# Performance work log

Measured on AMD Instinct MI355X. Metric: run time of the kernel, lower is better.

The kernel has to match this reference:

```python
import jax, jax.numpy as jnp
import numpy as np

B, LQ, LK, D, H = 2, 1024, 1024, 1024, 16
DH = D // H


def setup_inputs() -> dict:
    key = jax.random.key(0)
    ks = jax.random.split(key, 14)
    s = 1.0 / np.sqrt(D)
    inp = {
        "q": jax.random.normal(ks[0], (B, LQ, D), jnp.float32),
        "k": jax.random.normal(ks[1], (B, LK, D), jnp.float32),
        "v": jax.random.normal(ks[2], (B, LK, D), jnp.float32),
        "Wq": jax.random.normal(ks[3], (D, D), jnp.float32) * s,
        "bq": jnp.zeros((D,), jnp.float32),
        "Wk": jax.random.normal(ks[4], (D, D), jnp.float32) * s,
        "bk": jnp.zeros((D,), jnp.float32),
        "Wv": jax.random.normal(ks[5], (D, D), jnp.float32) * s,
        "bv": jnp.zeros((D,), jnp.float32),
        "Wo": jax.random.normal(ks[6], (D, D), jnp.float32) * s,
        "bo": jnp.zeros((D,), jnp.float32),
        "logits_bias": jax.random.normal(ks[7], (B, LQ, LK), jnp.float32),
        "key_padding_mask": jax.random.randint(ks[8], (B, LK), 0, 2) > 0,
    }
    return inp


def _split_heads(x):
    b, l, _ = x.shape
    return x.reshape(b, l, H, DH).transpose(0, 2, 1, 3)  # [B,H,L,DH]


def reference(q, k, v, Wq, bq, Wk, bk, Wv, bv, Wo, bo, logits_bias, key_padding_mask):
    qh = _split_heads(q @ Wq.T + bq)  # [B,H,Lq,DH]
    kh = _split_heads(k @ Wk.T + bk)  # [B,H,Lk,DH]
    vh = _split_heads(v @ Wv.T + bv)  # [B,H,Lk,DH]

    neg = jnp.finfo(qh.dtype).min
    # attn_mask = logits_bias broadcast over heads, masked_fill at padded keys
    attn_mask = jnp.where(key_padding_mask[:, None, None, :],
                          neg, logits_bias[:, None, :, :])  # [B,1,Lq,Lk]

    scale = 1.0 / np.sqrt(DH)
    scores = jnp.einsum('bhqd,bhkd->bhqk', qh, kh) * scale + attn_mask
    probs = jax.nn.softmax(scores, axis=-1)
    out = jnp.einsum('bhqk,bhkd->bhqd', probs, vh)  # [B,H,Lq,DH]
    out = out.transpose(0, 2, 1, 3).reshape(q.shape[0], q.shape[1], D)
    return out @ Wo.T + bo
```

## Files before the change

### kernel.cpp

```cpp
#include <hip/hip_runtime.h>


typedef _Float16 half8 __attribute__((ext_vector_type(8)));
typedef _Float16 half4_t __attribute__((ext_vector_type(4)));
typedef float f32x4 __attribute__((ext_vector_type(4)));

#define MFMA16(a, b, c) __builtin_amdgcn_mfma_f32_16x16x32_f16((a), (b), (c), 0, 0, 0)

#define WAITCNT_VM(n) asm volatile("s_waitcnt vmcnt(" #n ")" ::: "memory")
#define WAITCNT_LGKM0() asm volatile("s_waitcnt lgkmcnt(0)" ::: "memory")
#define RAW_BARRIER() asm volatile("s_barrier" ::: "memory")
#define EXP2F(x) __builtin_amdgcn_exp2f(x)

__device__ __forceinline__ void gload16(const void* g, void* l) {
  __builtin_amdgcn_global_load_lds(
      (const __attribute__((address_space(1))) unsigned int*)g,
      (__attribute__((address_space(3))) unsigned int*)l, 16, 0, 0);
}

__device__ __forceinline__ half8 frag_ld(const _Float16* t, int row, int ck) {
  return *(const half8*)(t + row * 64 + (((ck ^ (row & 7)) << 3)));
}

__global__ __launch_bounds__(256) void cvt_f32_f16(
    const float* __restrict__ q, const float* __restrict__ k, const float* __restrict__ v,
    const float* __restrict__ Wq, const float* __restrict__ Wk,
    const float* __restrict__ Wv, const float* __restrict__ Wo,
    const float* __restrict__ biasL, const int* __restrict__ kpm,
    _Float16* __restrict__ q16, _Float16* __restrict__ k16, _Float16* __restrict__ v16,
    _Float16* __restrict__ w16, _Float16* __restrict__ biasC) {
  const int y = blockIdx.y;
  if (y == 5) {
    const size_t i = ((size_t)blockIdx.x * 256 + threadIdx.x) * 8;
    const int b = (int)(i >> 20);
    const int kk = (int)(i & 1023);
    const int* mrow = kpm + (b << 10) + kk;
    const float4 b0 = *(const float4*)(biasL + i);
    const float4 b1 = *(const float4*)(biasL + i + 4);
    const int4 m0 = *(const int4*)mrow;
    const int4 m1 = *(const int4*)(mrow + 4);
    const float sc = 1.44269504f;
    half8 h;
    h[0] = m0.x ? (_Float16)-30000.f : (_Float16)(b0.x * sc - 8.f);
    h[1] = m0.y ? (_Float16)-30000.f : (_Float16)(b0.y * sc - 8.f);
    h[2] = m0.z ? (_Float16)-30000.f : (_Float16)(b0.z * sc - 8.f);
    h[3] = m0.w ? (_Float16)-30000.f : (_Float16)(b0.w * sc - 8.f);
    h[4] = m1.x ? (_Float16)-30000.f : (_Float16)(b1.x * sc - 8.f);
    h[5] = m1.y ? (_Float16)-30000.f : (_Float16)(b1.y * sc - 8.f);
    h[6] = m1.z ? (_Float16)-30000.f : (_Float16)(b1.z * sc - 8.f);
    h[7] = m1.w ? (_Float16)-30000.f : (_Float16)(b1.w * sc - 8.f);
    *(half8*)(biasC + i) = h;
    return;
  }
  const float* s;
  _Float16* d;
  const size_t M = (size_t)1024 * 1024;
  int x = blockIdx.x;
  switch (y) {
    case 0: s = q;  d = q16; break;
    case 1: s = k;  d = k16; break;
    case 2: s = v;  d = v16; break;
    case 3: if (x < 512) { s = Wq; d = w16; } else { s = Wk; d = w16 + M; x -= 512; } break;
    default: if (x < 512) { s = Wv; d = w16 + 2 * M; } else { s = Wo; d = w16 + 3 * M; x -= 512; } break;
  }
  const size_t i = ((size_t)x * 256 + threadIdx.x) * 8;
  const float4 a = *(const float4*)(s + i);
  const float4 bvv = *(const float4*)(s + i + 4);
  half8 h;
  h[0] = (_Float16)a.x; h[1] = (_Float16)a.y; h[2] = (_Float16)a.z; h[3] = (_Float16)a.w;
  h[4] = (_Float16)bvv.x; h[5] = (_Float16)bvv.y; h[6] = (_Float16)bvv.z; h[7] = (_Float16)bvv.w;
  *(half8*)(d + i) = h;
}

__global__ __launch_bounds__(256, 2) void mmp_big(
    const _Float16* __restrict__ Aq, const _Float16* __restrict__ Ak,
    const _Float16* __restrict__ Av, const _Float16* __restrict__ W16,
    const float* __restrict__ c0, const float* __restrict__ c1,
    const float* __restrict__ c2, _Float16* __restrict__ Dq,
    _Float16* __restrict__ Dk, _Float16* __restrict__ Dvt) {
  __shared__ __align__(16) _Float16 lds[32768];

  const int tid = threadIdx.x;
  const int wv = tid >> 6, ln = tid & 63;
  const int quad = ln >> 4, col = ln & 15;
  const int wm = wv >> 1, wn = wv & 1;
  const int n0 = blockIdx.x * 128;
  const int m0 = blockIdx.y * 128;
  const int z = blockIdx.z;
  const bool swapped = (z < 2);

  const _Float16* A = (z == 0) ? Aq : (z == 1) ? Ak : Av;
  const _Float16* Bw = W16 + (size_t)z * 1024 * 1024;
  const float* bias = (z == 0) ? c0 : (z == 1) ? c1 : c2;

  auto stage = [&](int buf, int k0) {
#pragma unroll
    for (int j = 0; j < 8; ++j) {
      const int ci = j * 256 + tid;
      const _Float16* src;
      if (ci < 1024) {
        const int row = ci >> 3, lc = (ci & 7) ^ (row & 7);
        src = A + (size_t)(m0 + row) * 1024 + k0 + lc * 8;
      } else {
        const int di = ci - 1024;
        const int row = di >> 3, lc = (di & 7) ^ (row & 7);
        src = Bw + (size_t)(n0 + row) * 1024 + k0 + lc * 8;
      }
      gload16(src, lds + buf * 16384 + (j * 256 + wv * 64) * 8);
    }
  };

  const f32x4 zero4 = {0.f, 0.f, 0.f, 0.f};
  f32x4 acc[4][4];
#pragma unroll
  for (int i = 0; i < 4; ++i)
#pragma unroll
    for (int j = 0; j < 4; ++j) acc[i][j] = zero4;

  auto kstep = [&](const _Float16* As, const _Float16* Bs) {
    half8 af0[4], bf0[4], af1[4], bf1[4];
#pragma unroll
    for (int mi = 0; mi < 4; ++mi) af0[mi] = frag_ld(As, wm * 64 + mi * 16 + col, quad);
#pragma unroll
    for (int ni = 0; ni < 4; ++ni) bf0[ni] = frag_ld(Bs, wn * 64 + ni * 16 + col, quad);
#pragma unroll
    for (int mi = 0; mi < 4; ++mi) af1[mi] = frag_ld(As, wm * 64 + mi * 16 + col, 4 + quad);
#pragma unroll
    for (int ni = 0; ni < 4; ++ni) bf1[ni] = frag_ld(Bs, wn * 64 + ni * 16 + col, 4 + quad);
    WAITCNT_LGKM0();
    RAW_BARRIER();
    if (swapped) {
#pragma unroll
      for (int ni = 0; ni < 4; ++ni)
#pragma unroll
        for (int mi = 0; mi < 4; ++mi)
          acc[ni][mi] = MFMA16(bf0[ni], af0[mi], acc[ni][mi]);
#pragma unroll
      for (int ni = 0; ni < 4; ++ni)
#pragma unroll
        for (int mi = 0; mi < 4; ++mi)
          acc[ni][mi] = MFMA16(bf1[ni], af1[mi], acc[ni][mi]);
    } else {
#pragma unroll
      for (int mi = 0; mi < 4; ++mi)
#pragma unroll
        for (int ni = 0; ni < 4; ++ni)
          acc[mi][ni] = MFMA16(af0[mi], bf0[ni], acc[mi][ni]);
#pragma unroll
      for (int mi = 0; mi < 4; ++mi)
#pragma unroll
        for (int ni = 0; ni < 4; ++ni)
          acc[mi][ni] = MFMA16(af1[mi], bf1[ni], acc[mi][ni]);
    }
  };

  stage(0, 0);
  for (int i = 0; i < 15; ++i) {
    stage((i + 1) & 1, (i + 1) * 64);
    WAITCNT_VM(8);
    RAW_BARRIER();
    kstep(lds + (i & 1) * 16384, lds + (i & 1) * 16384 + 8192);
  }
  WAITCNT_VM(0);
  RAW_BARRIER();
  kstep(lds + 16384, lds + 16384 + 8192);

  if (swapped) {
    float4 bv4[4];
#pragma unroll
    for (int ni = 0; ni < 4; ++ni)
      bv4[ni] = *(const float4*)&bias[n0 + wn * 64 + ni * 16 + quad * 4];
    _Float16* D = z ? Dk : Dq;
#pragma unroll
    for (int ni = 0; ni < 4; ++ni) {
      const int n_g = n0 + wn * 64 + ni * 16 + quad * 4;
      const int h = n_g >> 6, dh = n_g & 63;
#pragma unroll
      for (int mi = 0; mi < 4; ++mi) {
        const int m_g = m0 + wm * 64 + mi * 16 + col;
        const int b = m_g >> 10, l = m_g & 1023;
        half4_t st;
        st[0] = (_Float16)(acc[ni][mi][0] + bv4[ni].x);
        st[1] = (_Float16)(acc[ni][mi][1] + bv4[ni].y);
        st[2] = (_Float16)(acc[ni][mi][2] + bv4[ni].z);
        st[3] = (_Float16)(acc[ni][mi][3] + bv4[ni].w);
        *(half4_t*)&D[((size_t)((b * 16 + h) * 1024) + l) * 64 + dh] = st;
      }
    }
  } else {
    float bv[4];
#pragma unroll
    for (int ni = 0; ni < 4; ++ni) bv[ni] = bias[n0 + wn * 64 + ni * 16 + col];
    __syncthreads();
    _Float16* Ct = lds;
#pragma unroll
    for (int mi = 0; mi < 4; ++mi) {
      const int ml = wm * 64 + mi * 16 + quad * 4;
#pragma unroll
      for (int ni = 0; ni < 4; ++ni) {
        const int nl = wn * 64 + ni * 16 + col;
        half4_t h;
#pragma unroll
        for (int r = 0; r < 4; ++r) h[r] = (_Float16)(acc[mi][ni][r] + bv[ni]);
        *(half4_t*)(Ct + (size_t)nl * 136 + ml) = h;
      }
    }
    __syncthreads();
#pragma unroll
    for (int it = 0; it < 8; ++it) {
      const int ci = it * 256 + tid;
      const int n = ci >> 4;
      const int mc = (ci & 15) * 8;
      const half8 hv = *(const half8*)(Ct + (size_t)n * 136 + mc);
      const int n_g = n0 + n;
      const int h = n_g >> 6, dh = n_g & 63;
      const int m_g = m0 + mc;
      const int b = m_g >> 10, l = m_g & 1023;
      *(half8*)(Dvt + ((size_t)((b * 16 + h) * 64 + dh)) * 1024 + l) = hv;
    }
  }
}

__global__ __launch_bounds__(256) void mmp_final(
    const _Float16* __restrict__ A, const _Float16* __restrict__ Bw,
    const float* __restrict__ bias, float* __restrict__ Df) {
  __shared__ __align__(16) _Float16 lds[24576];

  const int tid = threadIdx.x;
  const int wv = tid >> 6, ln = tid & 63;
  const int quad = ln >> 4, col = ln & 15;
  const int wm = wv >> 1, wn = wv & 1;
  const int n0 = blockIdx.x * 128;
  const int m0 = blockIdx.y * 64;

  auto stage = [&](int buf, int k0) {
#pragma unroll
    for (int j = 0; j < 6; ++j) {
      const int ci = j * 256 + tid;
      const _Float16* src;
      if (ci < 512) {
        const int row = ci >> 3, lc = (ci & 7) ^ (row & 7);
        src = A + (size_t)(m0 + row) * 1024 + k0 + lc * 8;
      } else {
        const int di = ci - 512;
        const int row = di >> 3, lc = (di & 7) ^ (row & 7);
        src = Bw + (size_t)(n0 + row) * 1024 + k0 + lc * 8;
      }
      gload16(src, lds + buf * 12288 + (j * 256 + wv * 64) * 8);
    }
  };

  const f32x4 zero4 = {0.f, 0.f, 0.f, 0.f};
  f32x4 acc[4][2];
#pragma unroll
  for (int i = 0; i < 4; ++i)
#pragma unroll
    for (int j = 0; j < 2; ++j) acc[i][j] = zero4;

  auto kstep = [&](const _Float16* As, const _Float16* Bs) {
    half8 af[2][2], bf[2][4];
#pragma unroll
    for (int kk = 0; kk < 2; ++kk) {
#pragma unroll
      for (int mi = 0; mi < 2; ++mi)
        af[kk][mi] = frag_ld(As, wm * 32 + mi * 16 + col, kk * 4 + quad);
#pragma unroll
      for (int ni = 0; ni < 4; ++ni)
        bf[kk][ni] = frag_ld(Bs, wn * 64 + ni * 16 + col, kk * 4 + quad);
    }
    WAITCNT_LGKM0();
    RAW_BARRIER();
#pragma unroll
    for (int kk = 0; kk < 2; ++kk)
#pragma unroll
      for (int ni = 0; ni < 4; ++ni)
#pragma unroll
        for (int mi = 0; mi < 2; ++mi)
          acc[ni][mi] = MFMA16(bf[kk][ni], af[kk][mi], acc[ni][mi]);
  };

  stage(0, 0);
  for (int i = 0; i < 15; ++i) {
    stage((i + 1) & 1, (i + 1) * 64);
    WAITCNT_VM(6);
    RAW_BARRIER();
    kstep(lds + (i & 1) * 12288, lds + (i & 1) * 12288 + 4096);
  }
  WAITCNT_VM(0);
  RAW_BARRIER();
  kstep(lds + 12288, lds + 12288 + 4096);

  float4 bv4[4];
#pragma unroll
  for (int ni = 0; ni < 4; ++ni)
    bv4[ni] = *(const float4*)&bias[n0 + wn * 64 + ni * 16 + quad * 4];
#pragma unroll
  for (int ni = 0; ni < 4; ++ni) {
    const int n_g = n0 + wn * 64 + ni * 16 + quad * 4;
#pragma unroll
    for (int mi = 0; mi < 2; ++mi) {
      const int m_g = m0 + wm * 32 + mi * 16 + col;
      float4 st;
      st.x = acc[ni][mi][0] + bv4[ni].x;
      st.y = acc[ni][mi][1] + bv4[ni].y;
      st.z = acc[ni][mi][2] + bv4[ni].z;
      st.w = acc[ni][mi][3] + bv4[ni].w;
      *(float4*)&Df[(size_t)m_g * 1024 + n_g] = st;
    }
  }
}

__global__ __launch_bounds__(512, 4) void attn(
    const _Float16* __restrict__ Qh, const _Float16* __restrict__ Kh,
    const _Float16* __restrict__ Vt, const _Float16* __restrict__ biasC,
    _Float16* __restrict__ AO) {
  __shared__ __align__(16) _Float16 KV[2 * 8192];
  __shared__ __align__(16) _Float16 Pt[8][512];

  const int tid = threadIdx.x;
  const int wv = tid >> 6, ln = tid & 63;
  const int quad = ln >> 4, col = ln & 15;
  const int qsub = wv >> 1, khalf = wv & 1;
  const int fid = blockIdx.x;
  const int xcd = fid & 7, g = fid >> 3;
  const int bh = (xcd << 2) | (g >> 4);
  const int q0 = (g & 15) * 64;
  const int b = bh >> 4, hh = bh & 15;
  const int qg = q0 + qsub * 16 + col;

  const _Float16* Qp = Qh + ((size_t)bh * 1024 + qg) * 64;
  const half8 bq0 = *(const half8*)(Qp + quad * 8);
  const half8 bq1 = *(const half8*)(Qp + 32 + quad * 8);
  WAITCNT_VM(0);

  const _Float16* biasRow = biasC + ((size_t)(b * 1024 + qg)) * 1024;

  auto stageKV = [&](int buf, int it) {
    const int koff = it * 64;
#pragma unroll
    for (int j = 0; j < 2; ++j) {
      const int ci = j * 512 + tid;
      const void* src;
      if (ci < 512) {
        const int row = ci >> 3, lc = (ci & 7) ^ (row & 7);
        src = Kh + ((size_t)bh * 1024 + koff + row) * 64 + lc * 8;
      } else {
        const int di = ci - 512;
        const int row = di >> 3, lc = (di & 7) ^ (row & 7);
        src = Vt + ((size_t)bh * 64 + row) * 1024 + koff + lc * 8;
      }
      gload16(src, KV + buf * 8192 + (j * 512 + wv * 64) * 8);
    }
  };
  auto loadBias = [&](int it, half4_t* bb) {
    const int koff = it * 64 + khalf * 32;
#pragma unroll
    for (int mi = 0; mi < 2; ++mi)
      bb[mi] = *(const half4_t*)&biasRow[koff + mi * 16 + quad * 4];
  };

  const f32x4 zero4 = {0.f, 0.f, 0.f, 0.f};
  f32x4 o[4];
#pragma unroll
  for (int ni = 0; ni < 4; ++ni) o[ni] = zero4;
  float l_i = 0.f;
  _Float16* Pw = Pt[wv];

  auto compute = [&](int buf, const half4_t* bb) {
    const _Float16* Ks = KV + buf * 8192;
    const _Float16* Vs = Ks + 4096;
    f32x4 s[2];
#pragma unroll
    for (int mi = 0; mi < 2; ++mi) {
      f32x4 a4 = zero4;
      a4 = MFMA16(frag_ld(Ks, khalf * 32 + mi * 16 + col, quad), bq0, a4);
      a4 = MFMA16(frag_ld(Ks, khalf * 32 + mi * 16 + col, 4 + quad), bq1, a4);
      s[mi] = a4;
    }
#pragma unroll
    for (int mi = 0; mi < 2; ++mi)
#pragma unroll
      for (int r = 0; r < 4; ++r) {
        const float p = EXP2F(s[mi][r] * 0.18033688f + (float)bb[mi][r]);
        s[mi][r] = p;
        l_i += p;
      }
#pragma unroll
    for (int mi = 0; mi < 2; ++mi) {
      half4_t h;
      h[0] = (_Float16)s[mi][0]; h[1] = (_Float16)s[mi][1];
      h[2] = (_Float16)s[mi][2]; h[3] = (_Float16)s[mi][3];
      const int kloc = mi * 16 + quad * 4;
      *(half4_t*)(Pw + col * 32 + ((((kloc >> 3) ^ (col & 3)) << 3) | (kloc & 7))) = h;
    }
    const half8 p0 = *(const half8*)(Pw + col * 32 + ((quad ^ (col & 3)) << 3));
#pragma unroll
    for (int ni = 0; ni < 4; ++ni)
      o[ni] = MFMA16(frag_ld(Vs, ni * 16 + col, khalf * 4 + quad), p0, o[ni]);
  };

  half4_t bbA[2], bbB[2];
  stageKV(0, 0);
  loadBias(0, bbA);
  for (int i = 0; i < 15; ++i) {
    stageKV((i + 1) & 1, i + 1);
    loadBias(i + 1, bbB);
    WAITCNT_VM(4);
    RAW_BARRIER();
    compute(i & 1, bbA);
    WAITCNT_LGKM0();
    RAW_BARRIER();
    bbA[0] = bbB[0]; bbA[1] = bbB[1];
  }
  WAITCNT_VM(0);
  RAW_BARRIER();
  compute(1, bbA);

  l_i += __shfl_xor(l_i, 16);
  l_i += __shfl_xor(l_i, 32);

  __syncthreads();
  f32x4* Ox = (f32x4*)&KV[0];
  float* MlS = (float*)&KV[8192];
  if (khalf == 1) {
#pragma unroll
    for (int ni = 0; ni < 4; ++ni) Ox[(qsub * 4 + ni) * 64 + ln] = o[ni];
    MlS[qsub * 64 + ln] = l_i;
  }
  __syncthreads();
  if (khalf == 0) {
    const float l2 = MlS[qsub * 64 + ln];
    const float inv = 1.0f / (l_i + l2);
#pragma unroll
    for (int ni = 0; ni < 4; ++ni) {
      const f32x4 o2 = Ox[(qsub * 4 + ni) * 64 + ln];
      half4_t h;
#pragma unroll
      for (int r = 0; r < 4; ++r)
        h[r] = (_Float16)((o[ni][r] + o2[r]) * inv);
      *(half4_t*)&AO[((size_t)(b * 1024 + qg)) * 1024 + hh * 64 + ni * 16 + quad * 4] = h;
    }
  }
}

extern "C" void kernel_launch(void* const* d_in, const int* in_sizes, int n_in,
                              void* d_out, int out_size, void* d_ws, size_t ws_size,
                              hipStream_t stream) {
  (void)in_sizes; (void)n_in; (void)out_size; (void)ws_size;
  const float* q = (const float*)d_in[0];
  const float* k = (const float*)d_in[1];
  const float* v = (const float*)d_in[2];
  const float* Wq = (const float*)d_in[3];
  const float* bq = (const float*)d_in[4];
  const float* Wk = (const float*)d_in[5];
  const float* bk = (const float*)d_in[6];
  const float* Wv = (const float*)d_in[7];
  const float* bv = (const float*)d_in[8];
  const float* Wo = (const float*)d_in[9];
  const float* bo = (const float*)d_in[10];
  const float* lb = (const float*)d_in[11];
  const int* kpm = (const int*)d_in[12];
  float* out = (float*)d_out;

  const size_t NT = (size_t)2 * 1024 * 1024;
  _Float16* q16 = (_Float16*)d_ws;
  _Float16* k16 = q16 + NT;
  _Float16* v16 = k16 + NT;
  _Float16* Qh = v16 + NT;
  _Float16* Kh = Qh + NT;
  _Float16* Vt = Kh + NT;
  _Float16* w16 = Vt + NT;
  _Float16* biasC = w16 + 4 * (NT / 2);
  _Float16* AO = q16;

  cvt_f32_f16<<<dim3(1024, 6), 256, 0, stream>>>(q, k, v, Wq, Wk, Wv, Wo, lb, kpm,
                                                 q16, k16, v16, w16, biasC);
  mmp_big<<<dim3(8, 16, 3), 256, 0, stream>>>(q16, k16, v16, w16, bq, bk, bv,
                                              Qh, Kh, Vt);
  attn<<<dim3(512), 512, 0, stream>>>(Qh, Kh, Vt, biasC, AO);
  mmp_final<<<dim3(8, 32), 256, 0, stream>>>(AO, w16 + 3 * NT / 2, bo, out);
}
```

Baseline: 167.1 us.

## Triple-buffer K/V staging with one barrier per step; build P fragment via shuffles

```diff
diff --git a/kernel.cpp b/kernel.cpp
--- a/kernel.cpp
+++ b/kernel.cpp
@@ -3,7 +3,9 @@
 
 typedef _Float16 half8 __attribute__((ext_vector_type(8)));
 typedef _Float16 half4_t __attribute__((ext_vector_type(4)));
+typedef __fp16 fp16x2 __attribute__((ext_vector_type(2)));
 typedef float f32x4 __attribute__((ext_vector_type(4)));
+typedef unsigned int u32;
 
 #define MFMA16(a, b, c) __builtin_amdgcn_mfma_f32_16x16x32_f16((a), (b), (c), 0, 0, 0)
 
@@ -314,8 +316,7 @@
     const _Float16* __restrict__ Qh, const _Float16* __restrict__ Kh,
     const _Float16* __restrict__ Vt, const _Float16* __restrict__ biasC,
     _Float16* __restrict__ AO) {
-  __shared__ __align__(16) _Float16 KV[2 * 8192];
-  __shared__ __align__(16) _Float16 Pt[8][512];
+  __shared__ __align__(16) _Float16 KV[3 * 8192];
 
   const int tid = threadIdx.x;
   const int wv = tid >> 6, ln = tid & 63;
@@ -364,7 +365,12 @@
 #pragma unroll
   for (int ni = 0; ni < 4; ++ni) o[ni] = zero4;
   float l_i = 0.f;
-  _Float16* Pw = Pt[wv];
+
+  auto pk = [](float a, float bb) -> u32 {
+    union { fp16x2 h; u32 u; } cv;
+    cv.h = __builtin_amdgcn_cvt_pkrtz(a, bb);
+    return cv.u;
+  };
 
   auto compute = [&](int buf, const half4_t* bb) {
     const _Float16* Ks = KV + buf * 8192;
@@ -385,36 +391,45 @@
         s[mi][r] = p;
         l_i += p;
       }
-#pragma unroll
-    for (int mi = 0; mi < 2; ++mi) {
-      half4_t h;
-      h[0] = (_Float16)s[mi][0]; h[1] = (_Float16)s[mi][1];
-      h[2] = (_Float16)s[mi][2]; h[3] = (_Float16)s[mi][3];
-      const int kloc = mi * 16 + quad * 4;
-      *(half4_t*)(Pw + col * 32 + ((((kloc >> 3) ^ (col & 3)) << 3) | (kloc & 7))) = h;
-    }
-    const half8 p0 = *(const half8*)(Pw + col * 32 + ((quad ^ (col & 3)) << 3));
+    const u32 X0 = pk(s[0][0], s[0][1]), X1 = pk(s[0][2], s[0][3]);
+    const u32 Y0 = pk(s[1][0], s[1][1]), Y1 = pk(s[1][2], s[1][3]);
+    const u32 tX0 = __shfl_xor(X0, 16), tX1 = __shfl_xor(X1, 16);
+    const u32 tY0 = __shfl_xor(Y0, 16), tY1 = __shfl_xor(Y1, 16);
+    const bool e = (quad & 1) == 0;
+    const u32 L0 = e ? X0 : tX0, L1 = e ? X1 : tX1, L2 = e ? tX0 : X0, L3 = e ? tX1 : X1;
+    const u32 H0 = e ? Y0 : tY0, H1 = e ? Y1 : tY1, H2 = e ? tY0 : Y0, H3 = e ? tY1 : Y1;
+    const bool lo2 = quad < 2;
+    const u32 W0 = lo2 ? H0 : L0, W1 = lo2 ? H1 : L1, W2 = lo2 ? H2 : L2, W3 = lo2 ? H3 : L3;
+    const u32 R0 = __shfl_xor(W0, 32), R1 = __shfl_xor(W1, 32);
+    const u32 R2 = __shfl_xor(W2, 32), R3 = __shfl_xor(W3, 32);
+    const bool mid = (quad == 1) || (quad == 2);
+    union { u32 u[4]; half8 h; } pf;
+    pf.u[0] = mid ? R0 : (lo2 ? L0 : H0);
+    pf.u[1] = mid ? R1 : (lo2 ? L1 : H1);
+    pf.u[2] = mid ? R2 : (lo2 ? L2 : H2);
+    pf.u[3] = mid ? R3 : (lo2 ? L3 : H3);
 #pragma unroll
     for (int ni = 0; ni < 4; ++ni)
-      o[ni] = MFMA16(frag_ld(Vs, ni * 16 + col, khalf * 4 + quad), p0, o[ni]);
+      o[ni] = MFMA16(frag_ld(Vs, ni * 16 + col, khalf * 4 + quad), pf.h, o[ni]);
   };
 
   half4_t bbA[2], bbB[2];
   stageKV(0, 0);
   loadBias(0, bbA);
+#pragma unroll 3
   for (int i = 0; i < 15; ++i) {
-    stageKV((i + 1) & 1, i + 1);
+    stageKV((i + 1) % 3, i + 1);
     loadBias(i + 1, bbB);
     WAITCNT_VM(4);
-    RAW_BARRIER();
-    compute(i & 1, bbA);
     WAITCNT_LGKM0();
     RAW_BARRIER();
+    compute(i % 3, bbA);
     bbA[0] = bbB[0]; bbA[1] = bbB[1];
   }
   WAITCNT_VM(0);
+  WAITCNT_LGKM0();
   RAW_BARRIER();
-  compute(1, bbA);
+  compute(0, bbA);
 
   l_i += __shfl_xor(l_i, 16);
   l_i += __shfl_xor(l_i, 32);
```

Result: no change. 169.4 us (+1.4%).
